# Kernel optimization log

Measured on AMD Instinct MI355X. Metric: run time of the kernel, lower is better.

Reference implementation:

```python
import jax, jax.numpy as jnp
import numpy as np

POOLING_RATE = 4
K = 16  # neighbor_num
EPS = 1e-5


def setup_inputs() -> dict:
    key = jax.random.key(0)
    ks = jax.random.split(key, 20)
    B, N, C, D = 8, 4096, 256, 64
    inp = {
        'vertices': jax.random.normal(ks[0], (B, 3, N), jnp.float32),
        'feature_map': jax.random.normal(ks[1], (B, C, N), jnp.float32),
        # pos_mlp: Conv2d(3,64) -> BN(64) -> LeakyReLU -> Conv2d(64,C)
        'pw1': jax.random.normal(ks[2], (64, 3), jnp.float32) * 0.2,
        'pb1': jax.random.normal(ks[3], (64,), jnp.float32) * 0.02,
        'bn1_g': 1.0 + 0.1 * jax.random.normal(ks[4], (64,), jnp.float32),
        'bn1_b': 0.02 * jax.random.normal(ks[5], (64,), jnp.float32),
        'bn1_m': 0.02 * jax.random.normal(ks[6], (64,), jnp.float32),
        'bn1_v': jnp.ones((64,), jnp.float32),
        'pw2': jax.random.normal(ks[7], (C, 64), jnp.float32) * 0.1,
        'pb2': jax.random.normal(ks[8], (C,), jnp.float32) * 0.02,
        # attn_mlp: Conv2d(C,D) -> BN(D) -> LeakyReLU -> Conv2d(D, 3+C)
        'aw1': jax.random.normal(ks[9], (D, C), jnp.float32) * 0.05,
        'ab1': jax.random.normal(ks[10], (D,), jnp.float32) * 0.02,
        'bn2_g': 1.0 + 0.1 * jax.random.normal(ks[11], (D,), jnp.float32),
        'bn2_b': 0.02 * jax.random.normal(ks[12], (D,), jnp.float32),
        'bn2_m': 0.02 * jax.random.normal(ks[13], (D,), jnp.float32),
        'bn2_v': jnp.ones((D,), jnp.float32),
        'aw2': jax.random.normal(ks[14], (3 + C, D), jnp.float32) * 0.1,
        'ab2': jax.random.normal(ks[15], (3 + C,), jnp.float32) * 0.02,
    }
    return inp


def _fps(xyz, npoint):
    # xyz: [B,N,3] -> indices [B,npoint], deterministic start at index 0
    B, N, _ = xyz.shape

    def body(carry, _):
        dist, far = carry
        centroid = jnp.take_along_axis(xyz, far[:, None, None], axis=1)  # [B,1,3]
        d = jnp.sum((xyz - centroid) ** 2, axis=-1)  # [B,N]
        dist = jnp.minimum(dist, d)
        nxt = jnp.argmax(dist, axis=1).astype(jnp.int32)
        return (dist, nxt), far

    init = (jnp.full((B, N), 1e10, xyz.dtype), jnp.zeros((B,), jnp.int32))
    _, idxs = jax.lax.scan(body, init, None, length=npoint)
    return idxs.T  # [B, npoint]


def _conv1x1(x, w, b):
    # x: [B,Cin,M,K], w: [Cout,Cin]
    return jnp.einsum('oc,bcmk->bomk', w, x) + b[None, :, None, None]


def _bn(x, g, b, m, v):
    s = g / jnp.sqrt(v + EPS)
    return (x - m[None, :, None, None]) * s[None, :, None, None] + b[None, :, None, None]


def _forward(vertices, feature_map, pw1, pb1, bn1_g, bn1_b, bn1_m, bn1_v, pw2, pb2,
             aw1, ab1, bn2_g, bn2_b, bn2_m, bn2_v, aw2, ab2):
    B, _, N = vertices.shape
    M = int(N / POOLING_RATE + 0.5)
    xyz = jnp.transpose(vertices, (0, 2, 1))  # [B,N,3]

    fps_idx = _fps(xyz, M)  # [B,M]
    key_point = jnp.take_along_axis(vertices, fps_idx[:, None, :], axis=2)      # [B,3,M]
    key_feat = jnp.take_along_axis(feature_map, fps_idx[:, None, :], axis=2)    # [B,C,M]

    # kNN of key points in full cloud: squared distances [B,M,N]
    key_xyz = jnp.transpose(key_point, (0, 2, 1))  # [B,M,3]
    sqr = (jnp.sum(key_xyz ** 2, -1)[:, :, None]
           + jnp.sum(xyz ** 2, -1)[:, None, :]
           - 2.0 * jnp.einsum('bmc,bnc->bmn', key_xyz, xyz))
    _, knn_idx = jax.lax.top_k(-sqr, K)  # [B,M,K]

    gather = jax.vmap(lambda v, i: v[:, i])  # v:[C,N], i:[M,K] -> [C,M,K]
    group_point = gather(vertices, knn_idx)     # [B,3,M,K]
    group_feat = gather(feature_map, knn_idx)   # [B,C,M,K]

    qk_rel = key_feat[:, :, :, None] - group_feat   # [B,C,M,K]
    pos_rel = key_point[:, :, :, None] - group_point  # [B,3,M,K]

    h = jax.nn.leaky_relu(_bn(_conv1x1(pos_rel, pw1, pb1), bn1_g, bn1_b, bn1_m, bn1_v), 0.2)
    pos_embedding = _conv1x1(h, pw2, pb2)  # [B,C,M,K]

    h2 = jax.nn.leaky_relu(_bn(_conv1x1(qk_rel + pos_embedding, aw1, ab1),
                               bn2_g, bn2_b, bn2_m, bn2_v), 0.2)
    sample_weight = jax.nn.softmax(_conv1x1(h2, aw2, ab2), axis=-1)  # [B,3+C,M,K]

    new_xyz_w = sample_weight[:, :3]
    new_feat_w = sample_weight[:, 3:]
    group_feat = group_feat + pos_embedding
    new_feat = jnp.einsum('bcmk,bcmk->bcm', new_feat_w, group_feat)   # [B,C,M]
    new_point = jnp.einsum('bcmk,bcmk->bcm', new_xyz_w, group_point)  # [B,3,M]
    # concatenate (new_point, new_feat) along channel for a single output
    return jnp.concatenate([new_point, new_feat], axis=1)  # [B,3+C,M]


def reference(vertices, feature_map, pw1, pb1, bn1_g, bn1_b, bn1_m, bn1_v, pw2, pb2,
              aw1, ab1, bn2_g, bn2_b, bn2_m, bn2_v, aw2, ab2):
    return _forward(vertices, feature_map, pw1, pb1, bn1_g, bn1_b, bn1_m, bn1_v, pw2, pb2,
                    aw1, ab1, bn2_g, bn2_b, bn2_m, bn2_v, aw2, ab2)
```

## Files before the change

kernel.cpp:

```cpp
#include <hip/hip_runtime.h>
#include <math.h>

#define BB 8
#define NN 4096
#define CC 256
#define DD 64
#define MM 1024
#define KNB 16
#define OC 259
#define CHUNK 128
#define NCHUNK 8

typedef unsigned long long ull;

#define GRID_MAIN 1032
#define GRID_AUX 2585
#define AUX_G2 512

__device__ __forceinline__ void g2_unit(
    int u, int tid, char* smem, const float* fm, const float* aw1,
    const float* g2v, const float* v2, float* G2) {
  float (*a_l)[68] = (float(*)[68])smem;
  float (*b_l)[68] = (float(*)[68])(smem + 64 * 68 * 4);
  int b = u >> 6;
  int n0 = (u & 63) * 64;
  int rr = tid >> 4, q4 = tid & 15;
  float s2v[4];
#pragma unroll
  for (int j = 0; j < 4; ++j)
    s2v[j] = g2v[q4 * 4 + j] * rsqrtf(v2[q4 * 4 + j] + 1e-5f);
  float acc[4][4];
#pragma unroll
  for (int q = 0; q < 4; ++q)
#pragma unroll
    for (int x = 0; x < 4; ++x) acc[q][x] = 0.f;
  for (int c0 = 0; c0 < 256; c0 += 64) {
    __syncthreads();
#pragma unroll
    for (int rep = 0; rep < 4; ++rep) {
      int cc = rr + rep * 16;
      *(float4*)&a_l[cc][q4 * 4] =
          *(const float4*)&fm[((size_t)b * CC + c0 + cc) * NN + n0 + q4 * 4];
      float bv[4];
#pragma unroll
      for (int j = 0; j < 4; ++j)
        bv[j] = aw1[(q4 * 4 + j) * 256 + c0 + cc] * s2v[j];
      *(float4*)&b_l[cc][q4 * 4] = make_float4(bv[0], bv[1], bv[2], bv[3]);
    }
    __syncthreads();
#pragma unroll 8
    for (int kk = 0; kk < 64; ++kk) {
      float4 a4 = *(const float4*)&a_l[kk][rr * 4];
      float4 b4 = *(const float4*)&b_l[kk][q4 * 4];
      float av[4] = {a4.x, a4.y, a4.z, a4.w};
#pragma unroll
      for (int q = 0; q < 4; ++q) {
        acc[q][0] += av[q] * b4.x;
        acc[q][1] += av[q] * b4.y;
        acc[q][2] += av[q] * b4.z;
        acc[q][3] += av[q] * b4.w;
      }
    }
  }
#pragma unroll
  for (int q = 0; q < 4; ++q)
    *(float4*)&G2[((size_t)b * NN + n0 + rr * 4 + q) * 64 + q4 * 4] =
        make_float4(acc[q][0], acc[q][1], acc[q][2], acc[q][3]);
}

__device__ __forceinline__ void prep_unit(
    int tid, const float* pw1, const float* pb1, const float* g1,
    const float* bb1, const float* m1, const float* v1, const float* pw2,
    const float* aw1, const float* g2v, const float* bb2, const float* m2,
    const float* v2, const float* aw2, const float* ab1, float* w1f,
    float* b1f, float* ab1f, float* pw2t, float* aw1t, float* aw2t) {
  if (tid < 64) {
    float s = g1[tid] * rsqrtf(v1[tid] + 1e-5f);
    w1f[tid * 4 + 0] = pw1[tid * 3 + 0] * s;
    w1f[tid * 4 + 1] = pw1[tid * 3 + 1] * s;
    w1f[tid * 4 + 2] = pw1[tid * 3 + 2] * s;
    w1f[tid * 4 + 3] = 0.f;
    b1f[tid] = (pb1[tid] - m1[tid]) * s + bb1[tid];
    float s2 = g2v[tid] * rsqrtf(v2[tid] + 1e-5f);
    ab1f[tid] = (ab1[tid] - m2[tid]) * s2 + bb2[tid];
  }
  for (int x = tid; x < 64 * 256; x += 256) {
    int i = x >> 8, c = x & 255;
    pw2t[x] = pw2[c * 64 + i];
  }
  for (int x = tid; x < 256 * 64; x += 256) {
    int c = x >> 6, d = x & 63;
    float s2 = g2v[d] * rsqrtf(v2[d] + 1e-5f);
    aw1t[x] = aw1[d * 256 + c] * s2;
  }
  for (int x = tid; x < 64 * OC; x += 256) {
    int i = x / OC, o = x % OC;
    aw2t[i * 260 + o] = aw2[o * 64 + i];
  }
}

__device__ __forceinline__ void w12_unit(
    int w, int tid, const float* pw2, const float* aw1, const float* g2v,
    const float* v2, float* W12t) {
  int i = tid & 63;
  int d = w * 4 + (tid >> 6);
  float s2 = g2v[d] * rsqrtf(v2[d] + 1e-5f);
  const float* arow = aw1 + d * 256;
  float s = 0.f;
#pragma unroll 4
  for (int c = 0; c < 256; ++c) s += pw2[c * 64 + i] * arow[c];
  W12t[i * 64 + d] = s * s2;
}

__device__ __forceinline__ void transpose_unit(
    int rb, int tid, char* smem, const float* fm, float* fm_t) {
  float (*tile)[65] = (float(*)[65])smem;
  int b = rb >> 8;
  int rem = rb & 255;
  int c0 = (rem >> 6) * 64;
  int n0 = (rem & 63) * 64;
  const float* src = fm + (size_t)b * CC * NN;
  float* dst = fm_t + (size_t)b * NN * CC;
  int tx = tid & 63, ty = tid >> 6;
  for (int r = ty; r < 64; r += 4)
    tile[r][tx] = src[(size_t)(c0 + r) * NN + n0 + tx];
  __syncthreads();
  for (int r = ty; r < 64; r += 4)
    dst[(size_t)(n0 + r) * CC + c0 + tx] = tile[tx][r];
}

__device__ __forceinline__ void knn_to_lds(
    int b, int m, int lane, float* dbuf, const float* verts,
    const int* fpsi, int* kidx) {
  const float* vb = verts + (size_t)b * 3 * NN;
  int jm = fpsi[b * MM + m];
  float kx = vb[jm], ky = vb[NN + jm], kz = vb[2 * NN + jm];
  float kn = kx * kx + ky * ky + kz * kz;
  float v1 = INFINITY, v2 = INFINITY;
  int i1 = -1, i2 = -1;
  for (int t = 0; t < 64; ++t) {
    int j = t * 64 + lane;
    float x = vb[j], y = vb[NN + j], z = vb[2 * NN + j];
    float xn = x * x + y * y + z * z;
    float d = kn + xn - 2.0f * (kx * x + ky * y + kz * z);
    dbuf[lane * 65 + t] = d;
    if (d < v1) { v2 = v1; i2 = i1; v1 = d; i1 = j; }
    else if (d < v2) { v2 = d; i2 = j; }
  }
  for (int it = 0; it < KNB; ++it) {
    float rv = v1;
    int ri = i1;
#pragma unroll
    for (int off = 32; off >= 1; off >>= 1) {
      float ov = __shfl_down(rv, off, 64);
      int oi = __shfl_down(ri, off, 64);
      if (ov < rv || (ov == rv && oi < ri)) { rv = ov; ri = oi; }
    }
    ri = __shfl(ri, 0, 64);
    if (lane == 0) kidx[it] = ri;
    if (i1 == ri) {
      dbuf[lane * 65 + (ri >> 6)] = INFINITY;
      v1 = v2; i1 = i2;
      v2 = INFINITY; i2 = -1;
      if (i1 < 0) {
        v1 = INFINITY; v2 = INFINITY; i1 = -1; i2 = -1;
        for (int t = 0; t < 64; ++t) {
          float d = dbuf[lane * 65 + t];
          int j = t * 64 + lane;
          if (d < v1) { v2 = v1; i2 = i1; v1 = d; i1 = j; }
          else if (d < v2) { v2 = d; i2 = j; }
        }
      }
    }
  }
}

struct FuseS {
  float W12_l[64][68];
  float h_l[16][68];
  float hT_l[64][20];
  float h2T_l[64][20];
  float vmp[4][64];
  float vm_l[64];
  float kfpb[256];
  float pb2_l[256];
  float gp[3][16];
  float kp[4];
  int kidx[16];
};

__device__ __forceinline__ void fuse_item(
    int b, int m, int tid, char* smem, const float* verts,
    const float* fm_t, const float* G2, const int* fpsi,
    const float* w1f, const float* b1f, const float* ab1f,
    const float* aw1t, const float* W12t, const float* pw2t,
    const float* pb2, const float* aw2t, const float* ab2, float* out) {
  FuseS* S = (FuseS*)smem;
  const float* vb = verts + (size_t)b * 3 * NN;
  const float* fb = fm_t + (size_t)b * NN * CC;

  if (tid < 64)
    knn_to_lds(b, m, tid, (float*)S->W12_l, verts, fpsi, S->kidx);
  __syncthreads();

  int jm = fpsi[b * MM + m];
  S->kfpb[tid] = fb[(size_t)jm * CC + tid] + pb2[tid];
  S->pb2_l[tid] = pb2[tid];
  if (tid < 3) S->kp[tid] = vb[tid * NN + jm];
  __syncthreads();

  if (tid < 48) {
    int c = tid >> 4, k = tid & 15;
    S->gp[c][k] = vb[c * NN + S->kidx[k]];
  }
  {
    int i = tid >> 4, d4 = tid & 15;
#pragma unroll
    for (int rep = 0; rep < 4; ++rep)
      *(float4*)&S->W12_l[i + rep * 16][d4 * 4] =
          *(const float4*)&W12t[(i + rep * 16) * 64 + d4 * 4];
  }
  {
    int d = tid & 63, part = tid >> 6;
    float acc = 0.f;
#pragma unroll 4
    for (int cc = 0; cc < 64; ++cc) {
      int c = part * 64 + cc;
      acc += aw1t[c * 64 + d] * S->kfpb[c];
    }
    S->vmp[part][d] = acc;
  }
  __syncthreads();
  if (tid < 64)
    S->vm_l[tid] = S->vmp[0][tid] + S->vmp[1][tid] + S->vmp[2][tid] +
                   S->vmp[3][tid] + ab1f[tid];

  {
    int d = tid & 63, part = tid >> 6;
    float wd0 = w1f[d * 4 + 0], wd1 = w1f[d * 4 + 1], wd2 = w1f[d * 4 + 2];
    float bd = b1f[d];
#pragma unroll
    for (int j = 0; j < 4; ++j) {
      int k = part * 4 + j;
      float hv = wd0 * (S->kp[0] - S->gp[0][k]) +
                 wd1 * (S->kp[1] - S->gp[1][k]) +
                 wd2 * (S->kp[2] - S->gp[2][k]) + bd;
      hv = (hv > 0.f) ? hv : 0.2f * hv;
      S->h_l[k][d] = hv;
      S->hT_l[d][k] = hv;
    }
  }
  __syncthreads();

  {
    int k = tid & 15, d2 = tid >> 4;
    float4 g4 =
        *(const float4*)&G2[((size_t)b * NN + S->kidx[k]) * 64 + d2 * 4];
    float a0 = 0.f, a1 = 0.f, a2 = 0.f, a3 = 0.f;
#pragma unroll 4
    for (int i = 0; i < 64; ++i) {
      float hv = S->h_l[k][i];
      float4 w4 = *(const float4*)&S->W12_l[i][d2 * 4];
      a0 += hv * w4.x; a1 += hv * w4.y; a2 += hv * w4.z; a3 += hv * w4.w;
    }
    float4 v4 = *(const float4*)&S->vm_l[d2 * 4];
    float r0 = v4.x - g4.x + a0;
    float r1 = v4.y - g4.y + a1;
    float r2 = v4.z - g4.z + a2;
    float r3 = v4.w - g4.w + a3;
    S->h2T_l[d2 * 4 + 0][k] = (r0 > 0.f) ? r0 : 0.2f * r0;
    S->h2T_l[d2 * 4 + 1][k] = (r1 > 0.f) ? r1 : 0.2f * r1;
    S->h2T_l[d2 * 4 + 2][k] = (r2 > 0.f) ? r2 : 0.2f * r2;
    S->h2T_l[d2 * 4 + 3][k] = (r3 > 0.f) ? r3 : 0.2f * r3;
  }
  __syncthreads();

  if (tid < 3) {
    float lg[16];
    float bias = ab2[tid];
#pragma unroll
    for (int k = 0; k < 16; ++k) lg[k] = bias;
    const float* wp = aw2t + tid;
    for (int i = 0; i < 64; ++i) {
      float wv = wp[i * 260];
      float4 ha = *(const float4*)&S->h2T_l[i][0];
      float4 hb = *(const float4*)&S->h2T_l[i][4];
      float4 hc = *(const float4*)&S->h2T_l[i][8];
      float4 hd = *(const float4*)&S->h2T_l[i][12];
      lg[0] += wv * ha.x;  lg[1] += wv * ha.y;  lg[2] += wv * ha.z;  lg[3] += wv * ha.w;
      lg[4] += wv * hb.x;  lg[5] += wv * hb.y;  lg[6] += wv * hb.z;  lg[7] += wv * hb.w;
      lg[8] += wv * hc.x;  lg[9] += wv * hc.y;  lg[10] += wv * hc.z; lg[11] += wv * hc.w;
      lg[12] += wv * hd.x; lg[13] += wv * hd.y; lg[14] += wv * hd.z; lg[15] += wv * hd.w;
    }
    float mx = lg[0];
#pragma unroll
    for (int k = 1; k < 16; ++k) mx = fmaxf(mx, lg[k]);
    float sum = 0.f;
#pragma unroll
    for (int k = 0; k < 16; ++k) { lg[k] = __expf(lg[k] - mx); sum += lg[k]; }
    float inv = 1.f / sum;
    float a2 = 0.f;
#pragma unroll
    for (int k = 0; k < 16; ++k) a2 += lg[k] * S->gp[tid][k];
    out[((size_t)b * OC + tid) * MM + m] = a2 * inv;
  }

  {
    int o = tid + 3;
    float gfv[16];
#pragma unroll
    for (int k = 0; k < 16; ++k)
      gfv[k] = fb[(size_t)S->kidx[k] * CC + tid];
    float lg[16];
    float bias = ab2[o];
#pragma unroll
    for (int k = 0; k < 16; ++k) lg[k] = bias;
    const float* wp = aw2t + o;
#pragma unroll 4
    for (int i = 0; i < 64; ++i) {
      float wv = wp[i * 260];
      float4 ha = *(const float4*)&S->h2T_l[i][0];
      float4 hb = *(const float4*)&S->h2T_l[i][4];
      float4 hc = *(const float4*)&S->h2T_l[i][8];
      float4 hd = *(const float4*)&S->h2T_l[i][12];
      lg[0] += wv * ha.x;  lg[1] += wv * ha.y;  lg[2] += wv * ha.z;  lg[3] += wv * ha.w;
      lg[4] += wv * hb.x;  lg[5] += wv * hb.y;  lg[6] += wv * hb.z;  lg[7] += wv * hb.w;
      lg[8] += wv * hc.x;  lg[9] += wv * hc.y;  lg[10] += wv * hc.z; lg[11] += wv * hc.w;
      lg[12] += wv * hd.x; lg[13] += wv * hd.y; lg[14] += wv * hd.z; lg[15] += wv * hd.w;
    }
    float mx = lg[0];
#pragma unroll
    for (int k = 1; k < 16; ++k) mx = fmaxf(mx, lg[k]);
    float sum = 0.f;
#pragma unroll
    for (int k = 0; k < 16; ++k) { lg[k] = __expf(lg[k] - mx); sum += lg[k]; }
    float inv = 1.f / sum;
#pragma unroll
    for (int k = 0; k < 16; ++k) lg[k] *= inv;
    float acc = 0.f;
#pragma unroll
    for (int k = 0; k < 16; ++k) acc += lg[k] * gfv[k];
    const float* pcol = pw2t + tid;
#pragma unroll 4
    for (int i = 0; i < 64; ++i) {
      float p = pcol[i * 256];
      float4 ha = *(const float4*)&S->hT_l[i][0];
      float4 hb = *(const float4*)&S->hT_l[i][4];
      float4 hc = *(const float4*)&S->hT_l[i][8];
      float4 hd = *(const float4*)&S->hT_l[i][12];
      float hw = lg[0] * ha.x + lg[1] * ha.y + lg[2] * ha.z + lg[3] * ha.w +
                 lg[4] * hb.x + lg[5] * hb.y + lg[6] * hb.z + lg[7] * hb.w +
                 lg[8] * hc.x + lg[9] * hc.y + lg[10] * hc.z + lg[11] * hc.w +
                 lg[12] * hd.x + lg[13] * hd.y + lg[14] * hd.z + lg[15] * hd.w;
      acc += p * hw;
    }
    out[((size_t)b * OC + o) * MM + m] = S->pb2_l[tid] + acc;
  }
}

__global__ __launch_bounds__(256, 3) void pipe(
    const float* __restrict__ verts, const float* __restrict__ fm,
    const float* __restrict__ pw1, const float* __restrict__ pb1,
    const float* __restrict__ g1, const float* __restrict__ bb1,
    const float* __restrict__ m1, const float* __restrict__ v1,
    const float* __restrict__ pw2, const float* __restrict__ pb2,
    const float* __restrict__ aw1, const float* __restrict__ ab1,
    const float* __restrict__ g2v, const float* __restrict__ bb2,
    const float* __restrict__ m2, const float* __restrict__ v2,
    const float* __restrict__ aw2, const float* __restrict__ ab2,
    float* __restrict__ fm_t, float* __restrict__ G2,
    int* __restrict__ fpsi,
    float* __restrict__ w1f, float* __restrict__ b1f,
    float* __restrict__ ab1f, float* __restrict__ pw2t,
    float* __restrict__ aw1t, float* __restrict__ aw2t,
    float* __restrict__ W12t, float* __restrict__ dstate,
    int* __restrict__ fstate, float* __restrict__ out,
    int c_fps, int c_fuse, int aux_flag) {
  __shared__ __align__(16) char smem[49728];
  int blk = blockIdx.x;
  int tid = threadIdx.x;

  if (blk < 8) {
    if (c_fps < 0) return;
    float* lx = (float*)smem;
    float* ly = lx + NN;
    float* lz = ly + NN;
    ull* wres = (ull*)(lz + NN);
    int* fps_l = (int*)(wres + 8);
    int b = blk;
    const float* vb = verts + (size_t)b * 3 * NN;
    float px[16], py[16], pz[16], dist[16];
#pragma unroll
    for (int r = 0; r < 16; ++r) {
      int j = tid + r * 256;
      px[r] = vb[j]; py[r] = vb[NN + j]; pz[r] = vb[2 * NN + j];
      lx[j] = px[r]; ly[j] = py[r]; lz[j] = pz[r];
    }
    int far;
    if (c_fps == 0) {
#pragma unroll
      for (int r = 0; r < 16; ++r) dist[r] = 1e10f;
      far = 0;
    } else {
#pragma unroll
      for (int r = 0; r < 16; ++r)
        dist[r] = dstate[(size_t)b * NN + tid + r * 256];
      far = fstate[b];
    }
    __syncthreads();
    int s0 = c_fps * CHUNK, s1 = s0 + CHUNK;
    for (int s = s0; s < s1; ++s) {
      if (tid == 0) fps_l[s - s0] = far;
      if (s == MM - 1) break;
      float cx = lx[far], cy = ly[far], cz = lz[far];
      float vmax = -1.0f;
#pragma unroll
      for (int r = 0; r < 16; ++r) {
        float dx = px[r] - cx, dy = py[r] - cy, dz = pz[r] - cz;
        float d = dx * dx + dy * dy + dz * dz;
        dist[r] = fminf(dist[r], d);
        vmax = fmaxf(vmax, dist[r]);
      }
#define VRED(CTRL)                                                            \
      {                                                                       \
        int o = __builtin_amdgcn_update_dpp(__float_as_int(vmax),             \
                                            __float_as_int(vmax), CTRL, 0xF,  \
                                            0xF, false);                      \
        vmax = fmaxf(vmax, __int_as_float(o));                                \
      }
      VRED(0x111) VRED(0x112) VRED(0x114) VRED(0x118) VRED(0x142) VRED(0x143)
#undef VRED
      float svmax =
          __int_as_float(__builtin_amdgcn_readlane(__float_as_int(vmax), 63));
      int minj = 0x7FFFFFFF;
#pragma unroll
      for (int r = 0; r < 16; ++r) {
        int cand = (dist[r] == svmax) ? (tid + r * 256) : 0x7FFFFFFF;
        minj = (cand < minj) ? cand : minj;
      }
#define IRED(CTRL)                                                            \
      {                                                                       \
        int o = __builtin_amdgcn_update_dpp(minj, minj, CTRL, 0xF, 0xF,       \
                                            false);                          \
        minj = (o < minj) ? o : minj;                                         \
      }
      IRED(0x111) IRED(0x112) IRED(0x114) IRED(0x118) IRED(0x142) IRED(0x143)
#undef IRED
      if ((tid & 63) == 63)
        wres[(s & 1) * 4 + (tid >> 6)] =
            ((ull)(unsigned)__float_as_int(svmax) << 12) |
            (ull)(4095 - minj);
      __syncthreads();
      int p = s & 1;
      ull k0 = wres[p * 4 + 0], k1 = wres[p * 4 + 1];
      ull k2 = wres[p * 4 + 2], k3 = wres[p * 4 + 3];
      ull a = (k0 > k1) ? k0 : k1;
      ull c = (k2 > k3) ? k2 : k3;
      a = (c > a) ? c : a;
      far = 4095 - (int)(a & 0xFFFull);
    }
    __syncthreads();
    for (int x = tid; x < CHUNK; x += 256) fpsi[b * MM + s0 + x] = fps_l[x];
    if (s1 < MM) {
#pragma unroll
      for (int r = 0; r < 16; ++r)
        dstate[(size_t)b * NN + tid + r * 256] = dist[r];
      if (tid == 0) fstate[b] = far;
    }
    return;
  }

  if (aux_flag) {
    int u = blk - 8;
    if (u < AUX_G2) {
      g2_unit(u, tid, smem, fm, aw1, g2v, v2, G2);
    } else if (u == AUX_G2) {
      prep_unit(tid, pw1, pb1, g1, bb1, m1, v1, pw2, aw1, g2v, bb2, m2, v2,
                aw2, ab1, w1f, b1f, ab1f, pw2t, aw1t, aw2t);
    } else if (u < AUX_G2 + 17) {
      w12_unit(u - (AUX_G2 + 1), tid, pw2, aw1, g2v, v2, W12t);
    } else {
      transpose_unit(u - (AUX_G2 + 17), tid, smem, fm, fm_t);
    }
    return;
  }

  {
    if (c_fuse < 0) return;
    int e = blk - 8;
    int b = e & 7;
    int m = c_fuse * CHUNK + (e >> 3);
    fuse_item(b, m, tid, smem, verts, fm_t, G2, fpsi, w1f, b1f, ab1f,
              aw1t, W12t, pw2t, pb2, aw2t, ab2, out);
  }
}

extern "C" void kernel_launch(void* const* d_in, const int* in_sizes, int n_in,
                              void* d_out, int out_size, void* d_ws,
                              size_t ws_size, hipStream_t stream) {
  (void)in_sizes; (void)n_in; (void)out_size; (void)ws_size;
  const float* verts = (const float*)d_in[0];
  const float* fm = (const float*)d_in[1];
  const float* pw1 = (const float*)d_in[2];
  const float* pb1 = (const float*)d_in[3];
  const float* g1 = (const float*)d_in[4];
  const float* bb1 = (const float*)d_in[5];
  const float* m1 = (const float*)d_in[6];
  const float* v1 = (const float*)d_in[7];
  const float* pw2 = (const float*)d_in[8];
  const float* pb2 = (const float*)d_in[9];
  const float* aw1 = (const float*)d_in[10];
  const float* ab1 = (const float*)d_in[11];
  const float* g2 = (const float*)d_in[12];
  const float* bb2 = (const float*)d_in[13];
  const float* m2 = (const float*)d_in[14];
  const float* v2 = (const float*)d_in[15];
  const float* aw2 = (const float*)d_in[16];
  const float* ab2 = (const float*)d_in[17];
  float* out = (float*)d_out;

  char* ws = (char*)d_ws;
  float* fm_t = (float*)ws;
  float* G2 = (float*)(ws + 33554432);
  int* fpsi = (int*)(ws + 41943040);
  float* w1f = (float*)(ws + 42500096);
  float* b1f = w1f + 256;
  float* ab1f = b1f + 64;
  float* pw2t = ab1f + 64;
  float* aw1t = pw2t + 64 * 256;
  float* aw2t = aw1t + 256 * 64;
  float* W12t = aw2t + 64 * 260;
  float* dstate = (float*)(ws + 42715648);
  int* fstate = (int*)(ws + 42846720);

#define LAUNCH(grid, cf, cz, ax)                                              \
  hipLaunchKernelGGL(pipe, dim3(grid), dim3(256), 0, stream, verts, fm, pw1,  \
                     pb1, g1, bb1, m1, v1, pw2, pb2, aw1, ab1, g2, bb2, m2,   \
                     v2, aw2, ab2, fm_t, G2, fpsi, w1f, b1f, ab1f,            \
                     pw2t, aw1t, aw2t, W12t, dstate, fstate, out, cf, cz, ax)

  LAUNCH(GRID_AUX, 0, -1, 1);
  LAUNCH(GRID_MAIN, 1, 0, 0);
  LAUNCH(GRID_MAIN, 2, 1, 0);
  LAUNCH(GRID_MAIN, 3, 2, 0);
  LAUNCH(GRID_MAIN, 4, 3, 0);
  LAUNCH(GRID_MAIN, 5, 4, 0);
  LAUNCH(GRID_MAIN, 6, 5, 0);
  LAUNCH(GRID_MAIN, 7, 6, 0);
  LAUNCH(GRID_MAIN, -1, 7, 0);
#undef LAUNCH
}
```

Baseline: 1.012 ms.

## Parallelize per-point KNN search across all four waves of the block

The KNN selection for each sampled point previously ran on a single 64-lane wave while the other three waves idled. It now splits the 4096 candidate points across four waves, each keeping a local top-2 and a 16-entry distance buffer. A cross-wave reduction through shared memory with two block barriers per neighbour picks each of the K nearest. This cuts the serial scan length per lane by four but adds 32 block-level syncs per item.

```diff
diff --git a/kernel.cpp b/kernel.cpp
--- a/kernel.cpp
+++ b/kernel.cpp
@@ -129,21 +129,24 @@
     dst[(size_t)(n0 + r) * CC + c0 + tx] = tile[tx][r];
 }
 
-__device__ __forceinline__ void knn_to_lds(
-    int b, int m, int lane, float* dbuf, const float* verts,
-    const int* fpsi, int* kidx) {
+__device__ __forceinline__ void knn4(
+    int b, int m, int tid, float* dbuf, float* candv, int* candi,
+    int* kidx, const float* verts, const int* fpsi) {
+  int wave = tid >> 6, lane = tid & 63;
   const float* vb = verts + (size_t)b * 3 * NN;
   int jm = fpsi[b * MM + m];
   float kx = vb[jm], ky = vb[NN + jm], kz = vb[2 * NN + jm];
   float kn = kx * kx + ky * ky + kz * kz;
+  float* mybuf = dbuf + (wave * 64 + lane) * 17;
   float v1 = INFINITY, v2 = INFINITY;
   int i1 = -1, i2 = -1;
-  for (int t = 0; t < 64; ++t) {
-    int j = t * 64 + lane;
+#pragma unroll 4
+  for (int t = 0; t < 16; ++t) {
+    int j = (wave * 16 + t) * 64 + lane;
     float x = vb[j], y = vb[NN + j], z = vb[2 * NN + j];
     float xn = x * x + y * y + z * z;
     float d = kn + xn - 2.0f * (kx * x + ky * y + kz * z);
-    dbuf[lane * 65 + t] = d;
+    mybuf[t] = d;
     if (d < v1) { v2 = v1; i2 = i1; v1 = d; i1 = j; }
     else if (d < v2) { v2 = d; i2 = j; }
   }
@@ -156,17 +159,27 @@
       int oi = __shfl_down(ri, off, 64);
       if (ov < rv || (ov == rv && oi < ri)) { rv = ov; ri = oi; }
     }
-    ri = __shfl(ri, 0, 64);
-    if (lane == 0) kidx[it] = ri;
-    if (i1 == ri) {
-      dbuf[lane * 65 + (ri >> 6)] = INFINITY;
+    if (lane == 0) { candv[wave] = rv; candi[wave] = ri; }
+    __syncthreads();
+    float bv = candv[0];
+    int bi = candi[0];
+#pragma unroll
+    for (int w = 1; w < 4; ++w) {
+      float wv = candv[w];
+      int wi = candi[w];
+      if (wv < bv || (wv == bv && wi < bi)) { bv = wv; bi = wi; }
+    }
+    if (tid == 0) kidx[it] = bi;
+    __syncthreads();
+    if (i1 == bi) {
+      mybuf[(bi >> 6) & 15] = INFINITY;
       v1 = v2; i1 = i2;
       v2 = INFINITY; i2 = -1;
       if (i1 < 0) {
-        v1 = INFINITY; v2 = INFINITY; i1 = -1; i2 = -1;
-        for (int t = 0; t < 64; ++t) {
-          float d = dbuf[lane * 65 + t];
-          int j = t * 64 + lane;
+#pragma unroll 4
+        for (int t = 0; t < 16; ++t) {
+          float d = mybuf[t];
+          int j = (wave * 16 + t) * 64 + lane;
           if (d < v1) { v2 = v1; i2 = i1; v1 = d; i1 = j; }
           else if (d < v2) { v2 = d; i2 = j; }
         }
@@ -187,6 +200,8 @@
   float gp[3][16];
   float kp[4];
   int kidx[16];
+  float candv[4];
+  int candi[4];
 };
 
 __device__ __forceinline__ void fuse_item(
@@ -199,8 +214,8 @@
   const float* vb = verts + (size_t)b * 3 * NN;
   const float* fb = fm_t + (size_t)b * NN * CC;
 
-  if (tid < 64)
-    knn_to_lds(b, m, tid, (float*)S->W12_l, verts, fpsi, S->kidx);
+  knn4(b, m, tid, (float*)S->W12_l, S->candv, S->candi, S->kidx,
+       verts, fpsi);
   __syncthreads();
 
   int jm = fpsi[b * MM + m];
```

Measured after the change: 900.2 us. 11.0% less time.
